# Optimization experiments

Hardware: AMD Instinct MI355X
Metric: run time of the kernel (lower is better)

The kernel has to match this reference:

```python
import jax, jax.numpy as jnp
import numpy as np

B, H, S, D = 4, 16, 2048, 128

def setup_inputs() -> dict:
    key = jax.random.key(0)
    kk, kq, kv = jax.random.split(key, 3)
    k = jax.random.normal(kk, (B, H, S, D), dtype=jnp.float32)
    q = jax.random.normal(kq, (B, H, S, D), dtype=jnp.float32)
    v = jax.random.normal(kv, (B, H, S, D), dtype=jnp.float32)
    # causal mask: True = masked out (strictly upper triangle)
    mask = jnp.triu(jnp.ones((S, S), dtype=bool), k=1)
    return {"k": k, "q": q, "v": v, "mask": mask}

def reference(k, q, v, mask):
    d_k = k.shape[-1]
    # scores: [B, H, S, S]
    scores = jnp.einsum("bhqd,bhkd->bhqk", q, k) / jnp.sqrt(jnp.asarray(d_k, q.dtype))
    scores = jnp.where(mask, -jnp.inf, scores)
    # numerically stable softmax over last dim (matches manual max/exp/sum)
    p = jax.nn.softmax(scores, axis=-1)
    return jnp.einsum("bhqk,bhkd->bhqd", p, v)
```

## Files before the change

kernel.cpp:

```cpp
#include <hip/hip_runtime.h>
#include <hip/hip_bf16.h>
#include <math.h>

#define BATCH 4
#define HEADS 16
#define SEQ   2048
#define DIM   128
#define BHN   (BATCH*HEADS)

#define BQ 64
#define WQ 16
#define KT 32
#define NXB (SEQ/BQ)

typedef short bf16x8 __attribute__((ext_vector_type(8)));
typedef float f32x4  __attribute__((ext_vector_type(4)));

static __device__ __forceinline__ unsigned short f2bf(float f) {
    union { float f; unsigned u; } x; x.f = f;
    unsigned r = x.u + 0x7FFF + ((x.u >> 16) & 1);
    return (unsigned short)(r >> 16);
}

static __device__ __forceinline__ void async_cp16(const unsigned short* g, unsigned short* l) {
    __builtin_amdgcn_global_load_lds(
        (const __attribute__((address_space(1))) unsigned int*)g,
        (__attribute__((address_space(3))) unsigned int*)l,
        16, 0, 0);
}

__global__ __launch_bounds__(256) void cvt_kv(
    const float* __restrict__ k, const float* __restrict__ v,
    unsigned short* __restrict__ kb, unsigned short* __restrict__ vt) {
    __shared__ unsigned short T[DIM][72];
    const int bh = blockIdx.y;
    const int s0 = blockIdx.x * 64;
    const int t  = threadIdx.x;
    const long rbase = ((long)bh * SEQ + s0) * DIM;

    #pragma unroll
    for (int u = 0; u < 2; ++u) {
        long e = rbase + (long)(t + u * 256) * 16;
        const float* src = k + e;
        unsigned short* dst = kb + e;
        #pragma unroll
        for (int h = 0; h < 2; ++h) {
            float4 a0 = *(const float4*)(src + h * 8);
            float4 a1 = *(const float4*)(src + h * 8 + 4);
            union { uint4 u4; unsigned short s[8]; } p;
            p.s[0]=f2bf(a0.x); p.s[1]=f2bf(a0.y); p.s[2]=f2bf(a0.z); p.s[3]=f2bf(a0.w);
            p.s[4]=f2bf(a1.x); p.s[5]=f2bf(a1.y); p.s[6]=f2bf(a1.z); p.s[7]=f2bf(a1.w);
            *(uint4*)(dst + h * 8) = p.u4;
        }
    }
    {
        const int r = t >> 2, i = t & 3;
        const float* src = v + rbase + (long)r * DIM + i * 32;
        #pragma unroll
        for (int j = 0; j < 8; ++j) {
            float4 x = *(const float4*)(src + j * 4);
            const int d = i * 32 + j * 4;
            T[d + 0][r] = f2bf(x.x); T[d + 1][r] = f2bf(x.y);
            T[d + 2][r] = f2bf(x.z); T[d + 3][r] = f2bf(x.w);
        }
    }
    __syncthreads();
    {
        const int d = t >> 1, h = t & 1;
        unsigned short* dst = vt + ((long)bh * DIM + d) * SEQ + s0 + h * 32;
        #pragma unroll
        for (int m = 0; m < 4; ++m)
            *(uint4*)(dst + m * 8) = *(const uint4*)&T[d][h * 32 + m * 8];
    }
}

__global__ __launch_bounds__(256, 4) void attn_fwd(
    const float* __restrict__ qg,
    const unsigned short* __restrict__ kb,
    const unsigned short* __restrict__ vtg,
    float* __restrict__ out) {

    __shared__ unsigned short Kt[2][KT][DIM];
    __shared__ unsigned short Vt[2][DIM][KT];
    __shared__ unsigned short Pl[4][16][KT + 8];

    const int tid  = threadIdx.x;
    const int w    = tid >> 6;
    const int lane = tid & 63;
    const int quad = lane >> 4;
    const int ql   = lane & 15;

    const int flat = blockIdx.x;
    const int xcd  = flat & 7;
    const int slot = flat >> 3;
    const int bh   = (xcd << 3) | (slot & 7);
    const int shi  = slot >> 3;
    const int c_   = shi & 3;
    const int j_   = shi >> 2;
    const int xb   = (j_ & 1) ? (28 + c_ - 4 * j_) : (31 - c_ - 4 * j_);
    const int qb0 = xb * BQ;
    const int qw0 = qb0 + w * WQ;

    const long base = (long)bh * SEQ * DIM;
    const float scale = 0.08838834764831845f * 1.4426950408889634f;

    bf16x8 qf[4];
    {
        const float* qr = qg + base + (long)(qw0 + ql) * DIM;
        #pragma unroll
        for (int c = 0; c < 4; ++c) {
            const float* p = qr + c * 32 + quad * 8;
            float4 x = *(const float4*)(p);
            float4 y = *(const float4*)(p + 4);
            union { bf16x8 v; unsigned short s[8]; } u;
            u.s[0]=f2bf(x.x*scale); u.s[1]=f2bf(x.y*scale);
            u.s[2]=f2bf(x.z*scale); u.s[3]=f2bf(x.w*scale);
            u.s[4]=f2bf(y.x*scale); u.s[5]=f2bf(y.y*scale);
            u.s[6]=f2bf(y.z*scale); u.s[7]=f2bf(y.w*scale);
            qf[c] = u.v;
        }
    }

    f32x4 acc[8];
    #pragma unroll
    for (int n = 0; n < 8; ++n) acc[n] = (f32x4){0.f, 0.f, 0.f, 0.f};

    float m_ = -INFINITY;
    float l_ = 0.f;

    const unsigned short* kap[2];
    const unsigned short* vap[2];
    #pragma unroll
    for (int i = 0; i < 2; ++i) {
        const int idx = tid + i * 256;
        const int r   = idx >> 4;
        const int chg = (idx & 15) ^ (r & 15);
        kap[i] = kb + base + (long)r * DIM + chg * 8;
        const int d   = idx >> 2;
        const int cvg = (idx & 3) ^ ((d >> 1) & 3);
        vap[i] = vtg + base + (long)d * SEQ + cvg * 8;
    }
    const int ldso = ((tid >> 6) * 64) * 8;

    auto stage = [&](int buf) {
        #pragma unroll
        for (int i = 0; i < 2; ++i) {
            async_cp16(kap[i], &Kt[buf][0][0] + ldso + i * 2048);
            async_cp16(vap[i], &Vt[buf][0][0] + ldso + i * 2048);
            kap[i] += KT * DIM;
            vap[i] += KT;
        }
    };

    const int ntile = 2 * xb + 2;

    stage(0);

    for (int t = 0; t < ntile; ++t) {
        const int buf = t & 1;
        const int k0  = t * KT;
        __syncthreads();

        if (t + 1 < ntile) stage(buf ^ 1);

        if (k0 >= qw0 + WQ) continue;

        f32x4 sacc[2];
        sacc[0] = (f32x4){0.f, 0.f, 0.f, 0.f};
        sacc[1] = (f32x4){0.f, 0.f, 0.f, 0.f};
        __builtin_amdgcn_s_setprio(1);
        #pragma unroll
        for (int c = 0; c < 4; ++c) {
            const int sw = ((c * 4 + quad) ^ ql) * 8;
            bf16x8 kf0 = *(const bf16x8*)&Kt[buf][ql]     [sw];
            bf16x8 kf1 = *(const bf16x8*)&Kt[buf][16 + ql][sw];
            sacc[0] = __builtin_amdgcn_mfma_f32_16x16x32_bf16(kf0, qf[c], sacc[0], 0, 0, 0);
            sacc[1] = __builtin_amdgcn_mfma_f32_16x16x32_bf16(kf1, qf[c], sacc[1], 0, 0, 0);
        }
        __builtin_amdgcn_s_setprio(0);

        bf16x8 vf[8];
        #pragma unroll
        for (int n = 0; n < 8; ++n)
            vf[n] = *(const bf16x8*)&Vt[buf][n * 16 + ql][(quad ^ ((ql >> 1) & 3)) * 8];

        const int qrow   = qw0 + ql;
        const bool needm = (k0 + KT - 1 > qw0);
        float s[2][4];
        float tmax = -INFINITY;
        #pragma unroll
        for (int kk = 0; kk < 2; ++kk)
            #pragma unroll
            for (int r = 0; r < 4; ++r) {
                float sv = sacc[kk][r];
                if (needm) {
                    int kg = k0 + kk * 16 + quad * 4 + r;
                    sv = (kg <= qrow) ? sv : -INFINITY;
                }
                s[kk][r] = sv;
                tmax = fmaxf(tmax, sv);
            }
        tmax = fmaxf(tmax, __shfl_xor(tmax, 16));
        tmax = fmaxf(tmax, __shfl_xor(tmax, 32));

        const bool skip = __all(tmax <= m_ + 4.0f);
        const float mnew = skip ? m_ : fmaxf(m_, tmax);

        float rsum = 0.f;
        #pragma unroll
        for (int kk = 0; kk < 2; ++kk) {
            float p0 = __builtin_amdgcn_exp2f(s[kk][0] - mnew);
            float p1 = __builtin_amdgcn_exp2f(s[kk][1] - mnew);
            float p2 = __builtin_amdgcn_exp2f(s[kk][2] - mnew);
            float p3 = __builtin_amdgcn_exp2f(s[kk][3] - mnew);
            rsum += (p0 + p1) + (p2 + p3);
            union { uint2 u; __hip_bfloat162 h[2]; } pu;
            pu.h[0] = __float22bfloat162_rn(float2{p0, p1});
            pu.h[1] = __float22bfloat162_rn(float2{p2, p3});
            *(uint2*)&Pl[w][ql][kk * 16 + quad * 4] = pu.u;
        }
        rsum += __shfl_xor(rsum, 16);
        rsum += __shfl_xor(rsum, 32);

        float alpha;
        bool  resc;
        if (skip) {
            l_ += rsum;
            alpha = 1.f; resc = false;
        } else {
            alpha = __builtin_amdgcn_exp2f(m_ - mnew);
            l_ = l_ * alpha + rsum;
            m_ = mnew;
            resc = true;
        }

        if (resc) {
            #pragma unroll
            for (int r = 0; r < 4; ++r) {
                float ar = __shfl(alpha, quad * 4 + r);
                #pragma unroll
                for (int n = 0; n < 8; ++n) acc[n][r] *= ar;
            }
        }

        bf16x8 pf = *(const bf16x8*)&Pl[w][ql][quad * 8];
        __builtin_amdgcn_s_setprio(1);
        #pragma unroll
        for (int n = 0; n < 8; ++n)
            acc[n] = __builtin_amdgcn_mfma_f32_16x16x32_bf16(pf, vf[n], acc[n], 0, 0, 0);
        __builtin_amdgcn_s_setprio(0);
    }

    #pragma unroll
    for (int r = 0; r < 4; ++r) {
        float lr = __shfl(l_, quad * 4 + r);
        float il = 1.0f / lr;
        long orow = base + (long)(qw0 + quad * 4 + r) * DIM;
        #pragma unroll
        for (int n = 0; n < 8; ++n)
            out[orow + n * 16 + ql] = acc[n][r] * il;
    }
}

extern "C" void kernel_launch(void* const* d_in, const int* in_sizes, int n_in,
                              void* d_out, int out_size, void* d_ws, size_t ws_size,
                              hipStream_t stream) {
    const float* k = (const float*)d_in[0];
    const float* q = (const float*)d_in[1];
    const float* v = (const float*)d_in[2];
    float* o = (float*)d_out;

    unsigned short* kb = (unsigned short*)d_ws;
    unsigned short* vt = kb + (size_t)BHN * SEQ * DIM;

    cvt_kv<<<dim3(SEQ / 64, BHN), dim3(256), 0, stream>>>(k, v, kb, vt);

    attn_fwd<<<dim3(NXB * BHN), dim3(256), 0, stream>>>(q, kb, vt, o);
}
```

Before: 328.6 us.

## Transpose V in registers and unroll attention loop by two buffers

The V-transpose in the conversion kernel no longer goes through shared memory. Each thread loads a 4x8 block into registers and writes transposed bf16 pairs directly, and the K conversion now uses the packed bf16x2 intrinsic. In the attention kernel the double-buffered loop is unrolled by two so buffer indices are compile-time constants, and LDS addresses are precomputed as base pointers, which cuts per-iteration address arithmetic. The direct V stores are narrower (8-byte) strided writes, which may coalesce worse than the old LDS-staged 16-byte writes.

```diff
diff --git a/kernel.cpp b/kernel.cpp
--- a/kernel.cpp
+++ b/kernel.cpp
@@ -32,7 +32,6 @@
 __global__ __launch_bounds__(256) void cvt_kv(
     const float* __restrict__ k, const float* __restrict__ v,
     unsigned short* __restrict__ kb, unsigned short* __restrict__ vt) {
-    __shared__ unsigned short T[DIM][72];
     const int bh = blockIdx.y;
     const int s0 = blockIdx.x * 64;
     const int t  = threadIdx.x;
@@ -47,30 +46,34 @@
         for (int h = 0; h < 2; ++h) {
             float4 a0 = *(const float4*)(src + h * 8);
             float4 a1 = *(const float4*)(src + h * 8 + 4);
-            union { uint4 u4; unsigned short s[8]; } p;
-            p.s[0]=f2bf(a0.x); p.s[1]=f2bf(a0.y); p.s[2]=f2bf(a0.z); p.s[3]=f2bf(a0.w);
-            p.s[4]=f2bf(a1.x); p.s[5]=f2bf(a1.y); p.s[6]=f2bf(a1.z); p.s[7]=f2bf(a1.w);
-            *(uint4*)(dst + h * 8) = p.u4;
+            union { uint4 q; __hip_bfloat162 b[4]; } p;
+            p.b[0] = __float22bfloat162_rn(float2{a0.x, a0.y});
+            p.b[1] = __float22bfloat162_rn(float2{a0.z, a0.w});
+            p.b[2] = __float22bfloat162_rn(float2{a1.x, a1.y});
+            p.b[3] = __float22bfloat162_rn(float2{a1.z, a1.w});
+            *(uint4*)(dst + h * 8) = p.q;
         }
     }
     {
-        const int r = t >> 2, i = t & 3;
-        const float* src = v + rbase + (long)r * DIM + i * 32;
-        #pragma unroll
-        for (int j = 0; j < 8; ++j) {
-            float4 x = *(const float4*)(src + j * 4);
-            const int d = i * 32 + j * 4;
-            T[d + 0][r] = f2bf(x.x); T[d + 1][r] = f2bf(x.y);
-            T[d + 2][r] = f2bf(x.z); T[d + 3][r] = f2bf(x.w);
-        }
-    }
-    __syncthreads();
-    {
-        const int d = t >> 1, h = t & 1;
-        unsigned short* dst = vt + ((long)bh * DIM + d) * SEQ + s0 + h * 32;
-        #pragma unroll
-        for (int m = 0; m < 4; ++m)
-            *(uint4*)(dst + m * 8) = *(const uint4*)&T[d][h * 32 + m * 8];
+        const int rg = t & 15;
+        const int dg = t >> 4;
+        const float* src = v + rbase + (long)(rg * 4) * DIM + dg * 8;
+        float a[4][8];
+        #pragma unroll
+        for (int rr = 0; rr < 4; ++rr) {
+            float4 x = *(const float4*)(src + rr * DIM);
+            float4 y = *(const float4*)(src + rr * DIM + 4);
+            a[rr][0]=x.x; a[rr][1]=x.y; a[rr][2]=x.z; a[rr][3]=x.w;
+            a[rr][4]=y.x; a[rr][5]=y.y; a[rr][6]=y.z; a[rr][7]=y.w;
+        }
+        unsigned short* dstb = vt + ((long)bh * DIM + dg * 8) * SEQ + s0 + rg * 4;
+        #pragma unroll
+        for (int dd = 0; dd < 8; ++dd) {
+            union { uint2 u; __hip_bfloat162 b[2]; } p;
+            p.b[0] = __float22bfloat162_rn(float2{a[0][dd], a[1][dd]});
+            p.b[1] = __float22bfloat162_rn(float2{a[2][dd], a[3][dd]});
+            *(uint2*)(dstb + (long)dd * SEQ) = p.u;
+        }
     }
 }
 
@@ -128,61 +131,60 @@
     float m_ = -INFINITY;
     float l_ = 0.f;
 
-    const unsigned short* kap[2];
-    const unsigned short* vap[2];
+    int koff[2], voff[2];
     #pragma unroll
     for (int i = 0; i < 2; ++i) {
         const int idx = tid + i * 256;
         const int r   = idx >> 4;
         const int chg = (idx & 15) ^ (r & 15);
-        kap[i] = kb + base + (long)r * DIM + chg * 8;
+        koff[i] = r * DIM + chg * 8;
         const int d   = idx >> 2;
         const int cvg = (idx & 3) ^ ((d >> 1) & 3);
-        vap[i] = vtg + base + (long)d * SEQ + cvg * 8;
+        voff[i] = d * SEQ + cvg * 8;
     }
     const int ldso = ((tid >> 6) * 64) * 8;
-
-    auto stage = [&](int buf) {
+    const unsigned short* kbb = kb + base;
+    const unsigned short* vbb = vtg + base;
+
+    auto stage = [&](int buf, int k0s) {
+        const unsigned short* ku = kbb + k0s * DIM;
+        const unsigned short* vu = vbb + k0s;
         #pragma unroll
         for (int i = 0; i < 2; ++i) {
-            async_cp16(kap[i], &Kt[buf][0][0] + ldso + i * 2048);
-            async_cp16(vap[i], &Vt[buf][0][0] + ldso + i * 2048);
-            kap[i] += KT * DIM;
-            vap[i] += KT;
+            async_cp16(ku + koff[i], &Kt[buf][0][0] + ldso + i * 2048);
+            async_cp16(vu + voff[i], &Vt[buf][0][0] + ldso + i * 2048);
         }
     };
 
-    const int ntile = 2 * xb + 2;
-
-    stage(0);
-
-    for (int t = 0; t < ntile; ++t) {
-        const int buf = t & 1;
-        const int k0  = t * KT;
-        __syncthreads();
-
-        if (t + 1 < ntile) stage(buf ^ 1);
-
-        if (k0 >= qw0 + WQ) continue;
-
-        f32x4 sacc[2];
-        sacc[0] = (f32x4){0.f, 0.f, 0.f, 0.f};
-        sacc[1] = (f32x4){0.f, 0.f, 0.f, 0.f};
+    const unsigned short* kfb[4];
+    #pragma unroll
+    for (int c = 0; c < 4; ++c)
+        kfb[c] = &Kt[0][ql][((c * 4 + quad) ^ ql) * 8];
+    const unsigned short* vfb = &Vt[0][0][0] + ql * KT + (quad ^ ((ql >> 1) & 3)) * 8;
+    unsigned short* pwb = &Pl[w][ql][0];
+    const unsigned short* prb = &Pl[w][ql][quad * 8];
+
+    auto body = [&](const int buf, const int k0) {
+        if (k0 >= qw0 + WQ) return;
+        const int kbo = buf * (KT * DIM);
+        const int vbo = buf * (DIM * KT);
+
+        f32x4 sacc0 = (f32x4){0.f, 0.f, 0.f, 0.f};
+        f32x4 sacc1 = (f32x4){0.f, 0.f, 0.f, 0.f};
         __builtin_amdgcn_s_setprio(1);
         #pragma unroll
         for (int c = 0; c < 4; ++c) {
-            const int sw = ((c * 4 + quad) ^ ql) * 8;
-            bf16x8 kf0 = *(const bf16x8*)&Kt[buf][ql]     [sw];
-            bf16x8 kf1 = *(const bf16x8*)&Kt[buf][16 + ql][sw];
-            sacc[0] = __builtin_amdgcn_mfma_f32_16x16x32_bf16(kf0, qf[c], sacc[0], 0, 0, 0);
-            sacc[1] = __builtin_amdgcn_mfma_f32_16x16x32_bf16(kf1, qf[c], sacc[1], 0, 0, 0);
+            bf16x8 kf0 = *(const bf16x8*)(kfb[c] + kbo);
+            bf16x8 kf1 = *(const bf16x8*)(kfb[c] + kbo + 16 * DIM);
+            sacc0 = __builtin_amdgcn_mfma_f32_16x16x32_bf16(kf0, qf[c], sacc0, 0, 0, 0);
+            sacc1 = __builtin_amdgcn_mfma_f32_16x16x32_bf16(kf1, qf[c], sacc1, 0, 0, 0);
         }
         __builtin_amdgcn_s_setprio(0);
 
         bf16x8 vf[8];
         #pragma unroll
         for (int n = 0; n < 8; ++n)
-            vf[n] = *(const bf16x8*)&Vt[buf][n * 16 + ql][(quad ^ ((ql >> 1) & 3)) * 8];
+            vf[n] = *(const bf16x8*)(vfb + vbo + n * (16 * KT));
 
         const int qrow   = qw0 + ql;
         const bool needm = (k0 + KT - 1 > qw0);
@@ -192,7 +194,7 @@
         for (int kk = 0; kk < 2; ++kk)
             #pragma unroll
             for (int r = 0; r < 4; ++r) {
-                float sv = sacc[kk][r];
+                float sv = (kk ? sacc1 : sacc0)[r];
                 if (needm) {
                     int kg = k0 + kk * 16 + quad * 4 + r;
                     sv = (kg <= qrow) ? sv : -INFINITY;
@@ -217,7 +219,7 @@
             union { uint2 u; __hip_bfloat162 h[2]; } pu;
             pu.h[0] = __float22bfloat162_rn(float2{p0, p1});
             pu.h[1] = __float22bfloat162_rn(float2{p2, p3});
-            *(uint2*)&Pl[w][ql][kk * 16 + quad * 4] = pu.u;
+            *(uint2*)(pwb + kk * 16 + quad * 4) = pu.u;
         }
         rsum += __shfl_xor(rsum, 16);
         rsum += __shfl_xor(rsum, 32);
@@ -243,12 +245,26 @@
             }
         }
 
-        bf16x8 pf = *(const bf16x8*)&Pl[w][ql][quad * 8];
+        bf16x8 pf = *(const bf16x8*)prb;
         __builtin_amdgcn_s_setprio(1);
         #pragma unroll
         for (int n = 0; n < 8; ++n)
             acc[n] = __builtin_amdgcn_mfma_f32_16x16x32_bf16(pf, vf[n], acc[n], 0, 0, 0);
         __builtin_amdgcn_s_setprio(0);
+    };
+
+    const int ntile = 2 * xb + 2;
+
+    stage(0, 0);
+
+    for (int tt = 0; tt < ntile; tt += 2) {
+        __syncthreads();
+        if (tt + 1 < ntile) stage(1, (tt + 1) * KT);
+        body(0, tt * KT);
+
+        __syncthreads();
+        if (tt + 2 < ntile) stage(0, (tt + 2) * KT);
+        body(1, (tt + 1) * KT);
     }
 
     #pragma unroll
```

After: 321.8 us. 1.02x faster.
